# Kernel tuning notes

Measured on AMD Instinct MI355X. Metric: run time of the kernel, lower is better.

## Reference

```python
import jax, jax.numpy as jnp
import numpy as np

B, S = 64, 64
IMG_F, EMB, HID, VOCAB = 2048, 512, 512, 32000


def setup_inputs() -> dict:
    key = jax.random.key(0)
    ks = jax.random.split(key, 12)
    s = 0.02
    return {
        "img": jax.random.normal(ks[0], (B, IMG_F), jnp.float32),
        "captions": jax.random.randint(ks[1], (B, S), 0, VOCAB),
        "embed_W": jax.random.normal(ks[2], (VOCAB, EMB), jnp.float32) * s,
        "Wi": jax.random.normal(ks[3], (IMG_F, HID), jnp.float32) * s,
        "bi": jax.random.normal(ks[4], (HID,), jnp.float32) * s,
        "Wx": jax.random.normal(ks[5], (EMB, HID), jnp.float32) * s,
        "bx": jax.random.normal(ks[6], (HID,), jnp.float32) * s,
        "Wh": jax.random.normal(ks[7], (HID, HID), jnp.float32) * s,
        "bh": jax.random.normal(ks[8], (HID, HID)[:1] + (HID,), jnp.float32)[0] * s if False else jax.random.normal(ks[8], (HID,), jnp.float32) * s,
        "Wy": jax.random.normal(ks[9], (HID, VOCAB), jnp.float32) * s,
        "by": jax.random.normal(ks[10], (VOCAB,), jnp.float32) * s,
    }


def reference(img, captions, embed_W, Wi, bi, Wx, bx, Wh, bh, Wy, by):
    # Embed caption inputs (drop last token): (B, T, EMB), T = S-1
    x = embed_W[captions[:, :-1]]
    # Precompute input-to-hidden preactivations for all steps: (B, T, HID)
    pre = jnp.einsum("bte,eh->bth", x, Wx) + bx
    # Image features are injected only at t=0 (as in the torch loop)
    pre = pre.at[:, 0].add(img @ Wi + bi)

    def step(h_prev, p_t):
        h_t = jnp.tanh(p_t + h_prev @ Wh + bh)
        return h_t, h_t

    h0 = jnp.zeros((img.shape[0], Wh.shape[0]), dtype=x.dtype)
    _, hs = jax.lax.scan(step, h0, pre.transpose(1, 0, 2))  # (T, B, HID)
    hs = hs.transpose(1, 0, 2)  # (B, T, HID)
    # Output projection in one big GEMM (same math as per-step h2y)
    logits = jnp.einsum("bth,hv->btv", hs, Wy) + by  # (B, T, VOCAB)
    return logits
```

## Files before the change

### kernel.cpp

```cpp
#include <hip/hip_runtime.h>
#include <hip/hip_bf16.h>

#define B_    64
#define S_    64
#define T_    63
#define IMGF  2048
#define EMB   512
#define HID   512
#define VOCAB 32000
#define MROWS 4032
#define MPAD  4096

typedef __bf16 bf16;
typedef __bf16 bf16x8 __attribute__((ext_vector_type(8)));
typedef float  f32x4  __attribute__((ext_vector_type(4)));

__device__ __forceinline__ void gload_lds16(const void* g, void* l) {
  __builtin_amdgcn_global_load_lds(
      (const __attribute__((address_space(1))) unsigned int*)g,
      (__attribute__((address_space(3))) unsigned int*)l, 16, 0, 0);
}

#define LGKM_BARRIER() asm volatile("s_waitcnt lgkmcnt(0)\n\ts_barrier" ::: "memory")

__global__ __launch_bounds__(256) void transpose_w(
    const float* __restrict__ W, bf16* __restrict__ WT, int K, int N)
{
  __shared__ float tile[64][65];
  const int tx = threadIdx.x & 63, ty = threadIdx.x >> 6;
  const int n0 = blockIdx.x * 64, k0 = blockIdx.y * 64;
  #pragma unroll
  for (int r = ty; r < 64; r += 4)
    tile[r][tx] = W[(size_t)(k0 + r) * N + n0 + tx];
  __syncthreads();
  #pragma unroll
  for (int r = ty; r < 64; r += 4)
    WT[(size_t)(n0 + r) * K + k0 + tx] = (bf16)tile[tx][r];
}

__global__ __launch_bounds__(256) void transpose_wy_tiled(
    const float* __restrict__ W, bf16* __restrict__ T)
{
  __shared__ float tile[64][65];
  const int tx = threadIdx.x & 63, ty = threadIdx.x >> 6;
  const int n0 = blockIdx.x * 64, k0 = blockIdx.y * 64;
  #pragma unroll
  for (int r = ty; r < 64; r += 4)
    tile[r][tx] = W[(size_t)(k0 + r) * VOCAB + n0 + tx];
  __syncthreads();
  #pragma unroll
  for (int r = ty; r < 64; r += 4) {
    const int n = n0 + r, k = k0 + tx;
    const int bn = n >> 8, rr = n & 255, kt = k >> 5;
    const int sl = ((k & 31) >> 3) ^ ((rr >> 1) & 3);
    const size_t dst = (((size_t)(bn * 16 + kt) * 1024 + rr * 4 + sl) << 3)
                     + (k & 7);
    T[dst] = (bf16)tile[tx][r];
  }
}

__global__ __launch_bounds__(256) void embed_gather(
    const float* __restrict__ embW, const int* __restrict__ captions,
    bf16* __restrict__ X)
{
  const int r = blockIdx.x;
  const int tid = threadIdx.x;
  if (r < MROWS) {
    const int b = r / T_, t = r % T_;
    const int idx = captions[b * S_ + t];
    float2 v = ((const float2*)(embW + (size_t)idx * EMB))[tid];
    X[(size_t)r * EMB + 2 * tid]     = (bf16)v.x;
    X[(size_t)r * EMB + 2 * tid + 1] = (bf16)v.y;
  } else {
    X[(size_t)r * EMB + 2 * tid]     = (bf16)0.f;
    X[(size_t)r * EMB + 2 * tid + 1] = (bf16)0.f;
  }
}

__global__ __launch_bounds__(256) void img_to_bf16(
    const float* __restrict__ img, bf16* __restrict__ imgB)
{
  const int r = blockIdx.x;
  const int tid = threadIdx.x;
  #pragma unroll
  for (int j = 0; j < 8; j++) {
    const int c = tid + j * 256;
    const float v = (r < B_) ? img[(size_t)r * IMGF + c] : 0.f;
    imgB[(size_t)r * IMGF + c] = (bf16)v;
  }
}

__global__ __launch_bounds__(256) void gemm_bt(
    const bf16* __restrict__ A, const bf16* __restrict__ BT,
    const float* __restrict__ bias, float* __restrict__ C,
    int Mvalid, int N, int K)
{
  __shared__ __align__(16) bf16 As[2][128 * 32];
  __shared__ __align__(16) bf16 Bs[2][128 * 32];
  const int tid  = threadIdx.x;
  const int wave = tid >> 6, lane = tid & 63;
  const int wm = wave >> 1, wn = wave & 1;
  const int bm = blockIdx.x, bn = blockIdx.y;
  const int lg = lane >> 4, lr = lane & 15;

  f32x4 acc[4][4];
  #pragma unroll
  for (int m = 0; m < 4; m++)
    #pragma unroll
    for (int n = 0; n < 4; n++) acc[m][n] = (f32x4){0.f, 0.f, 0.f, 0.f};

  const bf16* Abase = A  + (size_t)bm * 128 * K;
  const bf16* Bbase = BT + (size_t)bn * 128 * K;

  const int c0 = wave * 64 + lane;
  const int r0 = c0 >> 2,  sl0 = (c0 & 3) ^ ((r0 >> 1) & 3);
  const int c1 = 256 + c0;
  const int r1 = c1 >> 2,  sl1 = (c1 & 3) ^ ((r1 >> 1) & 3);

  const int NT = K >> 5;

#define STAGE_TILE(buf, kt)                                                   \
  do {                                                                        \
    gload_lds16(Abase + (size_t)r0 * K + (kt) + sl0 * 8,                      \
                &As[buf][(wave * 64) * 8]);                                   \
    gload_lds16(Abase + (size_t)r1 * K + (kt) + sl1 * 8,                      \
                &As[buf][(256 + wave * 64) * 8]);                             \
    gload_lds16(Bbase + (size_t)r0 * K + (kt) + sl0 * 8,                      \
                &Bs[buf][(wave * 64) * 8]);                                   \
    gload_lds16(Bbase + (size_t)r1 * K + (kt) + sl1 * 8,                      \
                &Bs[buf][(256 + wave * 64) * 8]);                             \
  } while (0)

  STAGE_TILE(0, 0);
  int cur = 0;
  for (int it = 0; it < NT; ++it) {
    __syncthreads();
    if (it + 1 < NT) STAGE_TILE(cur ^ 1, (it + 1) * 32);

    bf16x8 af[4], bfr[4];
    #pragma unroll
    for (int m = 0; m < 4; m++) {
      const int r = wm * 64 + m * 16 + lr;
      const int sp = lg ^ ((r >> 1) & 3);
      af[m] = *(const bf16x8*)&As[cur][r * 32 + sp * 8];
    }
    #pragma unroll
    for (int n = 0; n < 4; n++) {
      const int r = wn * 64 + n * 16 + lr;
      const int sp = lg ^ ((r >> 1) & 3);
      bfr[n] = *(const bf16x8*)&Bs[cur][r * 32 + sp * 8];
    }
    #pragma unroll
    for (int m = 0; m < 4; m++)
      #pragma unroll
      for (int n = 0; n < 4; n++)
        acc[m][n] = __builtin_amdgcn_mfma_f32_16x16x32_bf16(af[m], bfr[n], acc[m][n], 0, 0, 0);
    cur ^= 1;
  }
#undef STAGE_TILE

  const int row0 = bm * 128 + wm * 64 + (lane >> 4) * 4;
  const int col0 = bn * 128 + wn * 64 + lr;
  #pragma unroll
  for (int m = 0; m < 4; m++) {
    #pragma unroll
    for (int n = 0; n < 4; n++) {
      const int col = col0 + n * 16;
      const float bv = bias[col];
      #pragma unroll
      for (int q = 0; q < 4; q++) {
        const int row = row0 + m * 16 + q;
        if (row < Mvalid) C[(size_t)row * N + col] = acc[m][n][q] + bv;
      }
    }
  }
}

__global__ __launch_bounds__(512, 1) void gemm_bt256(
    const bf16* __restrict__ A, const bf16* __restrict__ Btile,
    const float* __restrict__ bias, float* __restrict__ C,
    int Mvalid, int N, int K)
{
  __shared__ __align__(16) bf16 sm[4][2][256 * 32];
  const int tid  = threadIdx.x;
  const int wave = tid >> 6, lane = tid & 63;
  const int wm = wave >> 2, wn = wave & 3;
  const int lg = lane >> 4, lr = lane & 15;

  const int id  = blockIdx.x;
  const int cpx = gridDim.x >> 3;
  const int swz = (id & 7) * cpx + (id >> 3);
  const int bm  = swz & 15, bn = swz >> 4;

  f32x4 acc[8][4];
  #pragma unroll
  for (int m = 0; m < 8; m++)
    #pragma unroll
    for (int n = 0; n < 4; n++) acc[m][n] = (f32x4){0.f, 0.f, 0.f, 0.f};

  const bf16* Abase = A + (size_t)bm * 256 * K;

  const int ca0 = tid,        ra0 = ca0 >> 2, sa0 = (ca0 & 3) ^ ((ra0 >> 1) & 3);
  const int ca1 = tid + 512,  ra1 = ca1 >> 2, sa1 = (ca1 & 3) ^ ((ra1 >> 1) & 3);
  const int ldsb0 = (wave * 64) * 8;
  const int ldsb1 = (512 + wave * 64) * 8;

#define STAGE256(buf, kti)                                                    \
  do {                                                                        \
    const bf16* Bt_ = Btile + (((size_t)bn * 16 + (kti)) << 13);              \
    gload_lds16(Abase + (size_t)ra0 * K + (kti) * 32 + sa0 * 8,               \
                &sm[buf][0][ldsb0]);                                          \
    gload_lds16(Abase + (size_t)ra1 * K + (kti) * 32 + sa1 * 8,               \
                &sm[buf][0][ldsb1]);                                          \
    gload_lds16(Bt_ + (size_t)tid * 8,         &sm[buf][1][ldsb0]);           \
    gload_lds16(Bt_ + (size_t)(tid + 512) * 8, &sm[buf][1][ldsb1]);           \
  } while (0)

  const int NT = K >> 5;
  STAGE256(0, 0);
  STAGE256(1, 1);
  STAGE256(2, 2);

  #pragma unroll 1
  for (int it = 0; it < NT; ++it) {
    const int newer = (NT - 1 - it) > 2 ? 2 : (NT - 1 - it);
    switch (newer) {
      case 2:  asm volatile("s_waitcnt vmcnt(8)\n\ts_barrier" ::: "memory"); break;
      case 1:  asm volatile("s_waitcnt vmcnt(4)\n\ts_barrier" ::: "memory"); break;
      default: asm volatile("s_waitcnt vmcnt(0)\n\ts_barrier" ::: "memory"); break;
    }

    const bf16* As_ = sm[it & 3][0];
    const bf16* Bs_ = sm[it & 3][1];
    bf16x8 af[8], bfr[4];
    #pragma unroll
    for (int m = 0; m < 8; m++) {
      const int r = wm * 128 + m * 16 + lr;
      const int sp = lg ^ ((r >> 1) & 3);
      af[m] = *(const bf16x8*)&As_[(r * 4 + sp) * 8];
    }
    #pragma unroll
    for (int n = 0; n < 4; n++) {
      const int r = wn * 64 + n * 16 + lr;
      const int sp = lg ^ ((r >> 1) & 3);
      bfr[n] = *(const bf16x8*)&Bs_[(r * 4 + sp) * 8];
    }
    #pragma unroll
    for (int m = 0; m < 8; m++)
      #pragma unroll
      for (int n = 0; n < 4; n++)
        acc[m][n] = __builtin_amdgcn_mfma_f32_16x16x32_bf16(af[m], bfr[n], acc[m][n], 0, 0, 0);

    LGKM_BARRIER();
    if (it + 3 < NT) STAGE256((it + 3) & 3, it + 3);
  }
#undef STAGE256

  float* cst = (float*)&sm[0][0][0];
  float bvv[4];
  #pragma unroll
  for (int n = 0; n < 4; n++)
    bvv[n] = bias[bn * 256 + wn * 64 + n * 16 + lr];

  #pragma unroll
  for (int pass = 0; pass < 2; ++pass) {
    if (wm == pass) {
      #pragma unroll
      for (int m = 0; m < 8; m++)
        #pragma unroll
        for (int n = 0; n < 4; n++) {
          const int cc = wn * 64 + n * 16 + lr;
          #pragma unroll
          for (int q = 0; q < 4; q++)
            cst[(m * 16 + lg * 4 + q) * 256 + cc] = acc[m][n][q] + bvv[n];
        }
    }
    __syncthreads();
    const int rbase = bm * 256 + pass * 128;
    #pragma unroll
    for (int i = 0; i < 16; i++) {
      const int r = i * 8 + wave;
      const int grow = rbase + r;
      if (grow < Mvalid) {
        const f32x4 v = *(const f32x4*)&cst[r * 256 + lane * 4];
        *(f32x4*)&C[(size_t)grow * N + bn * 256 + lane * 4] = v;
      }
    }
    __syncthreads();
  }
}

#define FREG 48
#define FLDS 16
__global__ __launch_bounds__(512, 1) void rnn_reg8(
    const float* __restrict__ pre, const bf16* __restrict__ WhT,
    const float* __restrict__ bh, const float* __restrict__ pimg,
    bf16* __restrict__ hs)
{
  const int bg  = blockIdx.x;
  const int tid = threadIdx.x;
  const int wave = tid >> 6, lane = tid & 63;
  const int lg = lane >> 4, lr = lane & 15;
  const int gb0 = bg * 16;
  const int wc0 = wave * 64;

  __shared__ __align__(16) bf16 hsh[16 * 512];
  __shared__ __align__(16) bf16 bls[8 * FLDS * 64 * 8];

  bf16x8 bw[FREG];
  #pragma unroll
  for (int f = 0; f < 64; f++) {
    const int n = f >> 4, kf = f & 15;
    const bf16x8 v = *(const bf16x8*)(WhT + (size_t)(wc0 + n * 16 + lr) * 512
                                          + kf * 32 + lg * 8);
    if (f < FREG) bw[f] = v;
    else *(bf16x8*)&bls[((wave * FLDS + (f - FREG)) * 64 + lane) * 8] = v;
  }

  *(f32x4*)&hsh[tid * 16]     = (f32x4){0.f, 0.f, 0.f, 0.f};
  *(f32x4*)&hsh[tid * 16 + 8] = (f32x4){0.f, 0.f, 0.f, 0.f};

  float bhv[4];
  #pragma unroll
  for (int n = 0; n < 4; n++) bhv[n] = bh[wc0 + n * 16 + lr];
  const float* preb = pre + ((size_t)(gb0 + lg * 4) * T_) * 512 + wc0 + lr;

  __syncthreads();

  #pragma unroll 1
  for (int t = 0; t < T_; t++) {
    float prq[4][4];
    #pragma unroll
    for (int n = 0; n < 4; n++)
      #pragma unroll
      for (int q = 0; q < 4; q++)
        prq[n][q] = preb[(size_t)q * (T_ * 512) + (size_t)t * 512 + n * 16];

    f32x4 acc[4];
    #pragma unroll
    for (int n = 0; n < 4; n++) acc[n] = (f32x4){0.f, 0.f, 0.f, 0.f};

    #pragma unroll
    for (int kf = 0; kf < 16; kf++) {
      const int c = (kf * 4 + lg) ^ (lr & 7);
      const bf16x8 a = *(const bf16x8*)&hsh[(lr * 64 + c) * 8];
      #pragma unroll
      for (int n = 0; n < 4; n++) {
        const int f = n * 16 + kf;
        bf16x8 bfrag;
        if (f < FREG) bfrag = bw[f];
        else bfrag = *(const bf16x8*)&bls[((wave * FLDS + (f - FREG)) * 64 + lane) * 8];
        acc[n] = __builtin_amdgcn_mfma_f32_16x16x32_bf16(a, bfrag, acc[n], 0, 0, 0);
      }
    }
    LGKM_BARRIER();

    #pragma unroll
    for (int n = 0; n < 4; n++) {
      #pragma unroll
      for (int q = 0; q < 4; q++) {
        const int bl = lg * 4 + q;
        const int b  = gb0 + bl;
        const int k  = wc0 + n * 16 + lr;
        float s = acc[n][q] + prq[n][q] + bhv[n];
        if (t == 0) s += pimg[(size_t)b * HID + k];
        const float e = __builtin_exp2f(s * 2.885390081777927f);
        const float hv = 1.f - 2.f * __builtin_amdgcn_rcpf(e + 1.f);
        hs[((size_t)b * T_ + t) * HID + k] = (bf16)hv;
        const int c = (k >> 3) ^ (bl & 7);
        hsh[bl * 512 + c * 8 + (k & 7)] = (bf16)hv;
      }
    }
    LGKM_BARRIER();
  }
}

extern "C" void kernel_launch(void* const* d_in, const int* in_sizes, int n_in,
                              void* d_out, int out_size, void* d_ws, size_t ws_size,
                              hipStream_t stream) {
  const float* img      = (const float*)d_in[0];
  const int*   captions = (const int*)d_in[1];
  const float* embW     = (const float*)d_in[2];
  const float* Wi       = (const float*)d_in[3];
  const float* bi       = (const float*)d_in[4];
  const float* Wx       = (const float*)d_in[5];
  const float* bx       = (const float*)d_in[6];
  const float* Wh       = (const float*)d_in[7];
  const float* bh       = (const float*)d_in[8];
  const float* Wy       = (const float*)d_in[9];
  const float* by       = (const float*)d_in[10];
  float* logits = (float*)d_out;

  char* ws = (char*)d_ws;
  bf16*  WyT  = (bf16*)(ws);
  bf16*  WxT  = (bf16*)(ws + 32768000);
  bf16*  X    = (bf16*)(ws + 33292288);
  bf16*  hs   = (bf16*)(ws + 37486592);
  float* pre  = (float*)(ws + 41680896);
  float* pimg = (float*)(ws + 49938432);
  bf16*  imgB = (bf16*)(ws + 50200576);
  bf16*  WiT  = (bf16*)(ws + 50724864);
  bf16*  WhT  = WxT;

  transpose_wy_tiled<<<dim3(VOCAB / 64, HID / 64), 256, 0, stream>>>(Wy, WyT);
  transpose_w<<<dim3(HID / 64, EMB / 64), 256, 0, stream>>>(Wx, WxT, EMB, HID);
  transpose_w<<<dim3(HID / 64, IMGF / 64), 256, 0, stream>>>(Wi, WiT, IMGF, HID);
  img_to_bf16<<<128, 256, 0, stream>>>(img, imgB);

  embed_gather<<<MPAD, 256, 0, stream>>>(embW, captions, X);

  gemm_bt<<<dim3(MPAD / 128, HID / 128), 256, 0, stream>>>(X, WxT, bx, pre, MROWS, HID, HID);

  gemm_bt<<<dim3(1, HID / 128), 256, 0, stream>>>(imgB, WiT, bi, pimg, B_, HID, IMGF);

  transpose_w<<<dim3(HID / 64, HID / 64), 256, 0, stream>>>(Wh, WhT, HID, HID);

  hipMemsetAsync(hs + (size_t)MROWS * HID, 0,
                 (size_t)(MPAD - MROWS) * HID * sizeof(bf16), stream);

  rnn_reg8<<<4, 512, 0, stream>>>(pre, WhT, bh, pimg, hs);

  gemm_bt256<<<(MPAD / 256) * (VOCAB / 256), 512, 0, stream>>>(
      hs, WyT, by, logits, MROWS, VOCAB, HID);
}
```

Baseline: 587.8 us.

## Fuse RNN recurrence and output GEMM into persistent kernel with progress flags

Merges the sequential RNN kernel and the vocabulary projection GEMM into one persistent kernel. Four blocks run the recurrence and publish per-step progress counters, while the other blocks pull GEMM tiles from an atomic work queue and spin until the hidden rows for that tile exist. The hidden-state layout becomes time-major so each 256-row tile depends on only a few timesteps. This is meant to hide most of the large GEMM behind the serial recurrence. In exchange it adds spin-polling, atomic tile scheduling and a scattered output write pattern, and it relies on all 256 blocks being co-resident, otherwise it deadlocks.

```diff
diff --git a/kernel.cpp b/kernel.cpp
--- a/kernel.cpp
+++ b/kernel.cpp
@@ -10,6 +10,7 @@
 #define VOCAB 32000
 #define MROWS 4032
 #define MPAD  4096
+#define NTILES 2000
 
 typedef __bf16 bf16;
 typedef __bf16 bf16x8 __attribute__((ext_vector_type(8)));
@@ -176,203 +177,227 @@
   }
 }
 
-__global__ __launch_bounds__(512, 1) void gemm_bt256(
-    const bf16* __restrict__ A, const bf16* __restrict__ Btile,
-    const float* __restrict__ bias, float* __restrict__ C,
-    int Mvalid, int N, int K)
-{
-  __shared__ __align__(16) bf16 sm[4][2][256 * 32];
+#define FREG 48
+#define FLDS 16
+__global__ __launch_bounds__(512, 1) void rnn_gemm(
+    const float* __restrict__ pre, const bf16* __restrict__ WhT,
+    const float* __restrict__ bh, const float* __restrict__ pimg,
+    bf16* __restrict__ hs, const bf16* __restrict__ Btile,
+    const float* __restrict__ by, float* __restrict__ C,
+    unsigned* ctrl)
+{
+  __shared__ __align__(16) char smem[147456];
   const int tid  = threadIdx.x;
   const int wave = tid >> 6, lane = tid & 63;
+  const int lg = lane >> 4, lr = lane & 15;
+
+  if (blockIdx.x < 4) {
+    const int bg  = blockIdx.x;
+    const int gb0 = bg * 16;
+    const int wc0 = wave * 64;
+    bf16* hsh = (bf16*)smem;
+    bf16* bls = (bf16*)(smem + 16384);
+
+    bf16x8 bw[FREG];
+    #pragma unroll
+    for (int f = 0; f < 64; f++) {
+      const int n = f >> 4, kf = f & 15;
+      const bf16x8 v = *(const bf16x8*)(WhT + (size_t)(wc0 + n * 16 + lr) * 512
+                                            + kf * 32 + lg * 8);
+      if (f < FREG) bw[f] = v;
+      else *(bf16x8*)&bls[((wave * FLDS + (f - FREG)) * 64 + lane) * 8] = v;
+    }
+
+    *(f32x4*)&hsh[tid * 16]     = (f32x4){0.f, 0.f, 0.f, 0.f};
+    *(f32x4*)&hsh[tid * 16 + 8] = (f32x4){0.f, 0.f, 0.f, 0.f};
+
+    float bhv[4];
+    #pragma unroll
+    for (int n = 0; n < 4; n++) bhv[n] = bh[wc0 + n * 16 + lr];
+    const float* preb = pre + ((size_t)(gb0 + lg * 4) * T_) * 512 + wc0 + lr;
+
+    __syncthreads();
+
+    #pragma unroll 1
+    for (int t = 0; t < T_; t++) {
+      float prq[4][4];
+      #pragma unroll
+      for (int n = 0; n < 4; n++)
+        #pragma unroll
+        for (int q = 0; q < 4; q++)
+          prq[n][q] = preb[(size_t)q * (T_ * 512) + (size_t)t * 512 + n * 16];
+
+      f32x4 acc[4];
+      #pragma unroll
+      for (int n = 0; n < 4; n++) acc[n] = (f32x4){0.f, 0.f, 0.f, 0.f};
+
+      #pragma unroll
+      for (int kf = 0; kf < 16; kf++) {
+        const int c = (kf * 4 + lg) ^ (lr & 7);
+        const bf16x8 a = *(const bf16x8*)&hsh[(lr * 64 + c) * 8];
+        #pragma unroll
+        for (int n = 0; n < 4; n++) {
+          const int f = n * 16 + kf;
+          bf16x8 bfrag;
+          if (f < FREG) bfrag = bw[f];
+          else bfrag = *(const bf16x8*)&bls[((wave * FLDS + (f - FREG)) * 64 + lane) * 8];
+          acc[n] = __builtin_amdgcn_mfma_f32_16x16x32_bf16(a, bfrag, acc[n], 0, 0, 0);
+        }
+      }
+      LGKM_BARRIER();
+
+      #pragma unroll
+      for (int n = 0; n < 4; n++) {
+        #pragma unroll
+        for (int q = 0; q < 4; q++) {
+          const int bl = lg * 4 + q;
+          const int b  = gb0 + bl;
+          const int k  = wc0 + n * 16 + lr;
+          float s = acc[n][q] + prq[n][q] + bhv[n];
+          if (t == 0) s += pimg[(size_t)b * HID + k];
+          const float e = __builtin_exp2f(s * 2.885390081777927f);
+          const float hv = 1.f - 2.f * __builtin_amdgcn_rcpf(e + 1.f);
+          hs[((size_t)t * 64 + b) * HID + k] = (bf16)hv;
+          const int c = (k >> 3) ^ (bl & 7);
+          hsh[bl * 512 + c * 8 + (k & 7)] = (bf16)hv;
+        }
+      }
+      __syncthreads();
+      if (tid == 0)
+        __hip_atomic_store(&ctrl[bg], (unsigned)(t + 1),
+                           __ATOMIC_RELEASE, __HIP_MEMORY_SCOPE_AGENT);
+    }
+    __syncthreads();
+  }
+
+  bf16* base = (bf16*)smem;
+#define SMBUF(buf, op) (base + ((buf) * 2 + (op)) * 8192)
+  unsigned* idsl = (unsigned*)(smem + 131072);
+
   const int wm = wave >> 2, wn = wave & 3;
-  const int lg = lane >> 4, lr = lane & 15;
-
-  const int id  = blockIdx.x;
-  const int cpx = gridDim.x >> 3;
-  const int swz = (id & 7) * cpx + (id >> 3);
-  const int bm  = swz & 15, bn = swz >> 4;
-
-  f32x4 acc[8][4];
-  #pragma unroll
-  for (int m = 0; m < 8; m++)
-    #pragma unroll
-    for (int n = 0; n < 4; n++) acc[m][n] = (f32x4){0.f, 0.f, 0.f, 0.f};
-
-  const bf16* Abase = A + (size_t)bm * 256 * K;
 
   const int ca0 = tid,        ra0 = ca0 >> 2, sa0 = (ca0 & 3) ^ ((ra0 >> 1) & 3);
   const int ca1 = tid + 512,  ra1 = ca1 >> 2, sa1 = (ca1 & 3) ^ ((ra1 >> 1) & 3);
   const int ldsb0 = (wave * 64) * 8;
   const int ldsb1 = (512 + wave * 64) * 8;
 
+  for (;;) {
+    if (tid == 0) *idsl = atomicAdd(&ctrl[8], 1u);
+    __syncthreads();
+    const unsigned id = *idsl;
+    if (id >= (unsigned)NTILES) break;
+    const int bm = (int)(id / 125u), bn = (int)(id % 125u);
+
+    if (tid == 0) {
+      const unsigned tneed = (bm == 15) ? 63u : (unsigned)(4 * bm + 4);
+      #pragma unroll
+      for (int g = 0; g < 4; ++g) {
+        int poll = 0;
+        while (__hip_atomic_load(&ctrl[g], __ATOMIC_RELAXED,
+                                 __HIP_MEMORY_SCOPE_AGENT) < tneed) {
+          __builtin_amdgcn_s_sleep(8);
+          if ((++poll & 63) == 0)
+            (void)__hip_atomic_load(&ctrl[g], __ATOMIC_ACQUIRE,
+                                    __HIP_MEMORY_SCOPE_AGENT);
+        }
+      }
+    }
+    __syncthreads();
+    __builtin_amdgcn_fence(__ATOMIC_ACQUIRE, "agent");
+
+    const bf16* Abase = hs + (size_t)bm * 256 * 512;
+
+    f32x4 acc[8][4];
+    #pragma unroll
+    for (int m = 0; m < 8; m++)
+      #pragma unroll
+      for (int n = 0; n < 4; n++) acc[m][n] = (f32x4){0.f, 0.f, 0.f, 0.f};
+
 #define STAGE256(buf, kti)                                                    \
   do {                                                                        \
     const bf16* Bt_ = Btile + (((size_t)bn * 16 + (kti)) << 13);              \
-    gload_lds16(Abase + (size_t)ra0 * K + (kti) * 32 + sa0 * 8,               \
-                &sm[buf][0][ldsb0]);                                          \
-    gload_lds16(Abase + (size_t)ra1 * K + (kti) * 32 + sa1 * 8,               \
-                &sm[buf][0][ldsb1]);                                          \
-    gload_lds16(Bt_ + (size_t)tid * 8,         &sm[buf][1][ldsb0]);           \
-    gload_lds16(Bt_ + (size_t)(tid + 512) * 8, &sm[buf][1][ldsb1]);           \
+    gload_lds16(Abase + (size_t)ra0 * 512 + (kti) * 32 + sa0 * 8,             \
+                SMBUF(buf, 0) + ldsb0);                                       \
+    gload_lds16(Abase + (size_t)ra1 * 512 + (kti) * 32 + sa1 * 8,             \
+                SMBUF(buf, 0) + ldsb1);                                       \
+    gload_lds16(Bt_ + (size_t)tid * 8,         SMBUF(buf, 1) + ldsb0);        \
+    gload_lds16(Bt_ + (size_t)(tid + 512) * 8, SMBUF(buf, 1) + ldsb1);        \
   } while (0)
 
-  const int NT = K >> 5;
-  STAGE256(0, 0);
-  STAGE256(1, 1);
-  STAGE256(2, 2);
-
-  #pragma unroll 1
-  for (int it = 0; it < NT; ++it) {
-    const int newer = (NT - 1 - it) > 2 ? 2 : (NT - 1 - it);
-    switch (newer) {
-      case 2:  asm volatile("s_waitcnt vmcnt(8)\n\ts_barrier" ::: "memory"); break;
-      case 1:  asm volatile("s_waitcnt vmcnt(4)\n\ts_barrier" ::: "memory"); break;
-      default: asm volatile("s_waitcnt vmcnt(0)\n\ts_barrier" ::: "memory"); break;
-    }
-
-    const bf16* As_ = sm[it & 3][0];
-    const bf16* Bs_ = sm[it & 3][1];
-    bf16x8 af[8], bfr[4];
-    #pragma unroll
-    for (int m = 0; m < 8; m++) {
-      const int r = wm * 128 + m * 16 + lr;
-      const int sp = lg ^ ((r >> 1) & 3);
-      af[m] = *(const bf16x8*)&As_[(r * 4 + sp) * 8];
-    }
-    #pragma unroll
-    for (int n = 0; n < 4; n++) {
-      const int r = wn * 64 + n * 16 + lr;
-      const int sp = lg ^ ((r >> 1) & 3);
-      bfr[n] = *(const bf16x8*)&Bs_[(r * 4 + sp) * 8];
-    }
-    #pragma unroll
-    for (int m = 0; m < 8; m++)
-      #pragma unroll
-      for (int n = 0; n < 4; n++)
-        acc[m][n] = __builtin_amdgcn_mfma_f32_16x16x32_bf16(af[m], bfr[n], acc[m][n], 0, 0, 0);
-
-    LGKM_BARRIER();
-    if (it + 3 < NT) STAGE256((it + 3) & 3, it + 3);
-  }
-#undef STAGE256
-
-  float* cst = (float*)&sm[0][0][0];
-  float bvv[4];
-  #pragma unroll
-  for (int n = 0; n < 4; n++)
-    bvv[n] = bias[bn * 256 + wn * 64 + n * 16 + lr];
-
-  #pragma unroll
-  for (int pass = 0; pass < 2; ++pass) {
-    if (wm == pass) {
+    STAGE256(0, 0);
+    STAGE256(1, 1);
+    STAGE256(2, 2);
+
+    #pragma unroll 1
+    for (int it = 0; it < 16; ++it) {
+      const int newer = (15 - it) > 2 ? 2 : (15 - it);
+      switch (newer) {
+        case 2:  asm volatile("s_waitcnt vmcnt(8)\n\ts_barrier" ::: "memory"); break;
+        case 1:  asm volatile("s_waitcnt vmcnt(4)\n\ts_barrier" ::: "memory"); break;
+        default: asm volatile("s_waitcnt vmcnt(0)\n\ts_barrier" ::: "memory"); break;
+      }
+
+      const bf16* As_ = SMBUF(it & 3, 0);
+      const bf16* Bs_ = SMBUF(it & 3, 1);
+      bf16x8 af[8], bfr[4];
+      #pragma unroll
+      for (int m = 0; m < 8; m++) {
+        const int r = wm * 128 + m * 16 + lr;
+        const int sp = lg ^ ((r >> 1) & 3);
+        af[m] = *(const bf16x8*)&As_[(r * 4 + sp) * 8];
+      }
+      #pragma unroll
+      for (int n = 0; n < 4; n++) {
+        const int r = wn * 64 + n * 16 + lr;
+        const int sp = lg ^ ((r >> 1) & 3);
+        bfr[n] = *(const bf16x8*)&Bs_[(r * 4 + sp) * 8];
+      }
       #pragma unroll
       for (int m = 0; m < 8; m++)
         #pragma unroll
-        for (int n = 0; n < 4; n++) {
-          const int cc = wn * 64 + n * 16 + lr;
+        for (int n = 0; n < 4; n++)
+          acc[m][n] = __builtin_amdgcn_mfma_f32_16x16x32_bf16(af[m], bfr[n], acc[m][n], 0, 0, 0);
+
+      LGKM_BARRIER();
+      if (it + 3 < 16) STAGE256((it + 3) & 3, it + 3);
+    }
+#undef STAGE256
+
+    float* cst = (float*)smem;
+    float bvv[4];
+    #pragma unroll
+    for (int n = 0; n < 4; n++)
+      bvv[n] = by[bn * 256 + wn * 64 + n * 16 + lr];
+
+    #pragma unroll
+    for (int pass = 0; pass < 2; ++pass) {
+      if (wm == pass) {
+        #pragma unroll
+        for (int m = 0; m < 8; m++)
           #pragma unroll
-          for (int q = 0; q < 4; q++)
-            cst[(m * 16 + lg * 4 + q) * 256 + cc] = acc[m][n][q] + bvv[n];
+          for (int n = 0; n < 4; n++) {
+            const int cc = wn * 64 + n * 16 + lr;
+            #pragma unroll
+            for (int q = 0; q < 4; q++)
+              cst[(m * 16 + lg * 4 + q) * 256 + cc] = acc[m][n][q] + bvv[n];
+          }
+      }
+      __syncthreads();
+      const int rbase = bm * 256 + pass * 128;
+      #pragma unroll
+      for (int i = 0; i < 16; i++) {
+        const int r = i * 8 + wave;
+        const int grow = rbase + r;
+        const int tt = grow >> 6, bb = grow & 63;
+        if (tt < T_) {
+          const f32x4 v = *(const f32x4*)&cst[r * 256 + lane * 4];
+          *(f32x4*)&C[(size_t)(bb * T_ + tt) * VOCAB + bn * 256 + lane * 4] = v;
         }
-    }
-    __syncthreads();
-    const int rbase = bm * 256 + pass * 128;
-    #pragma unroll
-    for (int i = 0; i < 16; i++) {
-      const int r = i * 8 + wave;
-      const int grow = rbase + r;
-      if (grow < Mvalid) {
-        const f32x4 v = *(const f32x4*)&cst[r * 256 + lane * 4];
-        *(f32x4*)&C[(size_t)grow * N + bn * 256 + lane * 4] = v;
-      }
-    }
-    __syncthreads();
-  }
-}
-
-#define FREG 48
-#define FLDS 16
-__global__ __launch_bounds__(512, 1) void rnn_reg8(
-    const float* __restrict__ pre, const bf16* __restrict__ WhT,
-    const float* __restrict__ bh, const float* __restrict__ pimg,
-    bf16* __restrict__ hs)
-{
-  const int bg  = blockIdx.x;
-  const int tid = threadIdx.x;
-  const int wave = tid >> 6, lane = tid & 63;
-  const int lg = lane >> 4, lr = lane & 15;
-  const int gb0 = bg * 16;
-  const int wc0 = wave * 64;
-
-  __shared__ __align__(16) bf16 hsh[16 * 512];
-  __shared__ __align__(16) bf16 bls[8 * FLDS * 64 * 8];
-
-  bf16x8 bw[FREG];
-  #pragma unroll
-  for (int f = 0; f < 64; f++) {
-    const int n = f >> 4, kf = f & 15;
-    const bf16x8 v = *(const bf16x8*)(WhT + (size_t)(wc0 + n * 16 + lr) * 512
-                                          + kf * 32 + lg * 8);
-    if (f < FREG) bw[f] = v;
-    else *(bf16x8*)&bls[((wave * FLDS + (f - FREG)) * 64 + lane) * 8] = v;
-  }
-
-  *(f32x4*)&hsh[tid * 16]     = (f32x4){0.f, 0.f, 0.f, 0.f};
-  *(f32x4*)&hsh[tid * 16 + 8] = (f32x4){0.f, 0.f, 0.f, 0.f};
-
-  float bhv[4];
-  #pragma unroll
-  for (int n = 0; n < 4; n++) bhv[n] = bh[wc0 + n * 16 + lr];
-  const float* preb = pre + ((size_t)(gb0 + lg * 4) * T_) * 512 + wc0 + lr;
-
-  __syncthreads();
-
-  #pragma unroll 1
-  for (int t = 0; t < T_; t++) {
-    float prq[4][4];
-    #pragma unroll
-    for (int n = 0; n < 4; n++)
-      #pragma unroll
-      for (int q = 0; q < 4; q++)
-        prq[n][q] = preb[(size_t)q * (T_ * 512) + (size_t)t * 512 + n * 16];
-
-    f32x4 acc[4];
-    #pragma unroll
-    for (int n = 0; n < 4; n++) acc[n] = (f32x4){0.f, 0.f, 0.f, 0.f};
-
-    #pragma unroll
-    for (int kf = 0; kf < 16; kf++) {
-      const int c = (kf * 4 + lg) ^ (lr & 7);
-      const bf16x8 a = *(const bf16x8*)&hsh[(lr * 64 + c) * 8];
-      #pragma unroll
-      for (int n = 0; n < 4; n++) {
-        const int f = n * 16 + kf;
-        bf16x8 bfrag;
-        if (f < FREG) bfrag = bw[f];
-        else bfrag = *(const bf16x8*)&bls[((wave * FLDS + (f - FREG)) * 64 + lane) * 8];
-        acc[n] = __builtin_amdgcn_mfma_f32_16x16x32_bf16(a, bfrag, acc[n], 0, 0, 0);
-      }
-    }
-    LGKM_BARRIER();
-
-    #pragma unroll
-    for (int n = 0; n < 4; n++) {
-      #pragma unroll
-      for (int q = 0; q < 4; q++) {
-        const int bl = lg * 4 + q;
-        const int b  = gb0 + bl;
-        const int k  = wc0 + n * 16 + lr;
-        float s = acc[n][q] + prq[n][q] + bhv[n];
-        if (t == 0) s += pimg[(size_t)b * HID + k];
-        const float e = __builtin_exp2f(s * 2.885390081777927f);
-        const float hv = 1.f - 2.f * __builtin_amdgcn_rcpf(e + 1.f);
-        hs[((size_t)b * T_ + t) * HID + k] = (bf16)hv;
-        const int c = (k >> 3) ^ (bl & 7);
-        hsh[bl * 512 + c * 8 + (k & 7)] = (bf16)hv;
-      }
-    }
-    LGKM_BARRIER();
-  }
+      }
+      __syncthreads();
+    }
+  }
+#undef SMBUF
 }
 
 extern "C" void kernel_launch(void* const* d_in, const int* in_sizes, int n_in,
@@ -398,6 +423,7 @@
   bf16*  hs   = (bf16*)(ws + 37486592);
   float* pre  = (float*)(ws + 41680896);
   float* pimg = (float*)(ws + 49938432);
+  unsigned* ctrl = (unsigned*)(ws + 50069504);
   bf16*  imgB = (bf16*)(ws + 50200576);
   bf16*  WiT  = (bf16*)(ws + 50724864);
   bf16*  WhT  = WxT;
@@ -417,9 +443,7 @@
 
   hipMemsetAsync(hs + (size_t)MROWS * HID, 0,
                  (size_t)(MPAD - MROWS) * HID * sizeof(bf16), stream);
-
-  rnn_reg8<<<4, 512, 0, stream>>>(pre, WhT, bh, pimg, hs);
-
-  gemm_bt256<<<(MPAD / 256) * (VOCAB / 256), 512, 0, stream>>>(
-      hs, WyT, by, logits, MROWS, VOCAB, HID);
-}
+  hipMemsetAsync(ctrl, 0, 256, stream);
+
+  rnn_gemm<<<256, 512, 0, stream>>>(pre, WhT, bh, pimg, hs, WyT, by, logits, ctrl);
+}
```

After: 707.5 us. +20.4%, slower.

## Use K=64 tiles with double buffering in the vocab projection GEMM

Applied to the files above, without the earlier changes.

The big output-projection GEMM now stages 64-wide K tiles instead of 32-wide ones, with two LDS buffers instead of four. The Wy pre-tiling layout and the XOR swizzle change to match the 8-chunk rows. The loop is hardcoded to 8 iterations, which assumes K=512. The aim is to halve the number of barriers and waits per K and issue more MFMAs per sync, at the cost of a shallower prefetch pipeline.

```diff
diff --git a/kernel.cpp b/kernel.cpp
--- a/kernel.cpp
+++ b/kernel.cpp
@@ -51,9 +51,10 @@
   #pragma unroll
   for (int r = ty; r < 64; r += 4) {
     const int n = n0 + r, k = k0 + tx;
-    const int bn = n >> 8, rr = n & 255, kt = k >> 5;
-    const int sl = ((k & 31) >> 3) ^ ((rr >> 1) & 3);
-    const size_t dst = (((size_t)(bn * 16 + kt) * 1024 + rr * 4 + sl) << 3)
+    const int bn = n >> 8, rr = n & 255;
+    const int kt = k >> 6;
+    const int sl = ((k & 63) >> 3) ^ (rr & 7);
+    const size_t dst = (((size_t)(bn * 8 + kt) * 2048 + rr * 8 + sl) << 3)
                      + (k & 7);
     T[dst] = (bf16)tile[tx][r];
   }
@@ -181,7 +182,7 @@
     const float* __restrict__ bias, float* __restrict__ C,
     int Mvalid, int N, int K)
 {
-  __shared__ __align__(16) bf16 sm[4][2][256 * 32];
+  __shared__ __align__(16) bf16 sm[2][2][256 * 64];
   const int tid  = threadIdx.x;
   const int wave = tid >> 6, lane = tid & 63;
   const int wm = wave >> 2, wn = wave & 3;
@@ -200,61 +201,63 @@
 
   const bf16* Abase = A + (size_t)bm * 256 * K;
 
-  const int ca0 = tid,        ra0 = ca0 >> 2, sa0 = (ca0 & 3) ^ ((ra0 >> 1) & 3);
-  const int ca1 = tid + 512,  ra1 = ca1 >> 2, sa1 = (ca1 & 3) ^ ((ra1 >> 1) & 3);
-  const int ldsb0 = (wave * 64) * 8;
-  const int ldsb1 = (512 + wave * 64) * 8;
-
-#define STAGE256(buf, kti)                                                    \
+  int rs[4], ss[4];
+  #pragma unroll
+  for (int i = 0; i < 4; i++) {
+    const int c = tid + i * 512;
+    rs[i] = c >> 3;
+    ss[i] = (c & 7) ^ (rs[i] & 7);
+  }
+
+#define STAGE64(buf, kti)                                                     \
   do {                                                                        \
-    const bf16* Bt_ = Btile + (((size_t)bn * 16 + (kti)) << 13);              \
-    gload_lds16(Abase + (size_t)ra0 * K + (kti) * 32 + sa0 * 8,               \
-                &sm[buf][0][ldsb0]);                                          \
-    gload_lds16(Abase + (size_t)ra1 * K + (kti) * 32 + sa1 * 8,               \
-                &sm[buf][0][ldsb1]);                                          \
-    gload_lds16(Bt_ + (size_t)tid * 8,         &sm[buf][1][ldsb0]);           \
-    gload_lds16(Bt_ + (size_t)(tid + 512) * 8, &sm[buf][1][ldsb1]);           \
+    const bf16* Bt_ = Btile + (((size_t)(bn * 8 + (kti))) << 14);             \
+    _Pragma("unroll")                                                         \
+    for (int i = 0; i < 4; i++)                                               \
+      gload_lds16(Abase + (size_t)rs[i] * K + (kti) * 64 + ss[i] * 8,         \
+                  &sm[buf][0][(i * 512 + wave * 64) * 8]);                    \
+    _Pragma("unroll")                                                         \
+    for (int i = 0; i < 4; i++)                                               \
+      gload_lds16(Bt_ + (size_t)(tid + i * 512) * 8,                          \
+                  &sm[buf][1][(i * 512 + wave * 64) * 8]);                    \
   } while (0)
 
-  const int NT = K >> 5;
-  STAGE256(0, 0);
-  STAGE256(1, 1);
-  STAGE256(2, 2);
+  STAGE64(0, 0);
+  STAGE64(1, 1);
 
   #pragma unroll 1
-  for (int it = 0; it < NT; ++it) {
-    const int newer = (NT - 1 - it) > 2 ? 2 : (NT - 1 - it);
-    switch (newer) {
-      case 2:  asm volatile("s_waitcnt vmcnt(8)\n\ts_barrier" ::: "memory"); break;
-      case 1:  asm volatile("s_waitcnt vmcnt(4)\n\ts_barrier" ::: "memory"); break;
-      default: asm volatile("s_waitcnt vmcnt(0)\n\ts_barrier" ::: "memory"); break;
-    }
-
-    const bf16* As_ = sm[it & 3][0];
-    const bf16* Bs_ = sm[it & 3][1];
-    bf16x8 af[8], bfr[4];
-    #pragma unroll
-    for (int m = 0; m < 8; m++) {
-      const int r = wm * 128 + m * 16 + lr;
-      const int sp = lg ^ ((r >> 1) & 3);
-      af[m] = *(const bf16x8*)&As_[(r * 4 + sp) * 8];
-    }
-    #pragma unroll
-    for (int n = 0; n < 4; n++) {
-      const int r = wn * 64 + n * 16 + lr;
-      const int sp = lg ^ ((r >> 1) & 3);
-      bfr[n] = *(const bf16x8*)&Bs_[(r * 4 + sp) * 8];
-    }
-    #pragma unroll
-    for (int m = 0; m < 8; m++)
-      #pragma unroll
-      for (int n = 0; n < 4; n++)
-        acc[m][n] = __builtin_amdgcn_mfma_f32_16x16x32_bf16(af[m], bfr[n], acc[m][n], 0, 0, 0);
+  for (int it = 0; it < 8; ++it) {
+    if (it < 7) asm volatile("s_waitcnt vmcnt(8)\n\ts_barrier" ::: "memory");
+    else        asm volatile("s_waitcnt vmcnt(0)\n\ts_barrier" ::: "memory");
+
+    const bf16* As_ = sm[it & 1][0];
+    const bf16* Bs_ = sm[it & 1][1];
+    #pragma unroll
+    for (int kk = 0; kk < 2; kk++) {
+      bf16x8 af[8], bfr[4];
+      #pragma unroll
+      for (int m = 0; m < 8; m++) {
+        const int r = wm * 128 + m * 16 + lr;
+        const int sp = (kk * 4 + lg) ^ (r & 7);
+        af[m] = *(const bf16x8*)&As_[(r * 8 + sp) * 8];
+      }
+      #pragma unroll
+      for (int n = 0; n < 4; n++) {
+        const int r = wn * 64 + n * 16 + lr;
+        const int sp = (kk * 4 + lg) ^ (r & 7);
+        bfr[n] = *(const bf16x8*)&Bs_[(r * 8 + sp) * 8];
+      }
+      #pragma unroll
+      for (int m = 0; m < 8; m++)
+        #pragma unroll
+        for (int n = 0; n < 4; n++)
+          acc[m][n] = __builtin_amdgcn_mfma_f32_16x16x32_bf16(af[m], bfr[n], acc[m][n], 0, 0, 0);
+    }
 
     LGKM_BARRIER();
-    if (it + 3 < NT) STAGE256((it + 3) & 3, it + 3);
-  }
-#undef STAGE256
+    if (it + 2 < 8) STAGE64(it & 1, it + 2);
+  }
+#undef STAGE64
 
   float* cst = (float*)&sm[0][0][0];
   float bvv[4];
```

Result: no change. 589.3 us (+0.3%).
